# Optimization experiments

Hardware: AMD Instinct MI355X
Metric: run time of the kernel (lower is better)

The kernel has to match this reference:

```python
import jax, jax.numpy as jnp
import numpy as np
from jax import lax

NB_DIGITS = 2
BASE = 10
NUMS = BASE ** NB_DIGITS            # 100 possible values per number
SUMS = 2 * (NUMS - 1) + 1           # 199 possible sums (circuit roots)
B = 4096                            # logical batch size
N_IMAGES = B * 2 * NB_DIGITS        # 16384 digit images


def setup_inputs() -> dict:
    key = jax.random.key(0)
    ks = jax.random.split(key, 11)
    s = 0.1
    return {
        "images": jax.random.normal(ks[0], (N_IMAGES, 1, 28, 28), jnp.float32),
        "conv1_w": jax.random.normal(ks[1], (6, 1, 5, 5), jnp.float32) * s,
        "conv1_b": jax.random.normal(ks[2], (6,), jnp.float32) * s,
        "conv2_w": jax.random.normal(ks[3], (16, 6, 5, 5), jnp.float32) * s,
        "conv2_b": jax.random.normal(ks[4], (16,), jnp.float32) * s,
        "fc1_w": jax.random.normal(ks[5], (120, 256), jnp.float32) * s,
        "fc1_b": jax.random.normal(ks[6], (120,), jnp.float32) * s,
        "fc2_w": jax.random.normal(ks[7], (84, 120), jnp.float32) * s,
        "fc2_b": jax.random.normal(ks[8], (84,), jnp.float32) * s,
        "fc3_w": jax.random.normal(ks[9], (10, 84), jnp.float32) * s,
        "fc3_b": jax.random.normal(ks[10], (10,), jnp.float32) * s,
    }


def _conv(x, w, b):
    y = lax.conv_general_dilated(x, w, (1, 1), 'VALID',
                                 dimension_numbers=('NCHW', 'OIHW', 'NCHW'))
    return y + b[None, :, None, None]


def _maxpool2(x):
    return lax.reduce_window(x, -jnp.inf, lax.max, (1, 1, 2, 2), (1, 1, 2, 2), 'VALID')


def _lenet(x, c1w, c1b, c2w, c2b, f1w, f1b, f2w, f2b, f3w, f3b):
    x = jax.nn.relu(_maxpool2(_conv(x, c1w, c1b)))   # [N,6,12,12]
    x = jax.nn.relu(_maxpool2(_conv(x, c2w, c2b)))   # [N,16,4,4]
    x = x.reshape(-1, 16 * 4 * 4)
    x = jax.nn.relu(x @ f1w.T + f1b)
    x = jax.nn.relu(x @ f2w.T + f2b)
    x = x @ f3w.T + f3b
    return jax.nn.log_softmax(x, axis=-1)            # [N,10]


def _circuit(lp):
    # lp: [B, 2*NB_DIGITS, 10] per-digit log-probs.
    # Vars layout from get_circuit: positions 0..NB_DIGITS-1 = n1 digits (MSB first),
    # positions NB_DIGITS..2*NB_DIGITS-1 = n2 digits. Neg-literal weights are 0 in
    # log space (the `zeros` arg), so each model's weight = sum of digit log-probs;
    # OR over models = logsumexp grouped by n1+n2.
    d = jnp.arange(NUMS)
    hi, lo = d // BASE, d % BASE
    lp1 = lp[:, 0, hi] + lp[:, 1, lo]                # [B, NUMS] log P(n1=k)
    lp2 = lp[:, 2, hi] + lp[:, 3, lo]                # [B, NUMS] log P(n2=k)
    M = (lp1[:, :, None] + lp2[:, None, :]).reshape(lp.shape[0], -1)  # [B, NUMS^2]
    seg = (jnp.arange(NUMS)[:, None] + jnp.arange(NUMS)[None, :]).reshape(-1)
    Mf = M.T                                          # [NUMS^2, B]
    m = jax.ops.segment_max(Mf, seg, num_segments=SUMS)              # [SUMS, B]
    ssum = jax.ops.segment_sum(jnp.exp(Mf - m[seg]), seg, num_segments=SUMS)
    return (jnp.log(ssum) + m).T                      # [B, SUMS] log P(sum=s)


def reference(images, conv1_w, conv1_b, conv2_w, conv2_b,
              fc1_w, fc1_b, fc2_w, fc2_b, fc3_w, fc3_b):
    logp = _lenet(images, conv1_w, conv1_b, conv2_w, conv2_b,
                  fc1_w, fc1_b, fc2_w, fc2_b, fc3_w, fc3_b)   # [N_IMAGES,10]
    lp = logp.reshape(B, 2 * NB_DIGITS, BASE)
    return _circuit(lp)
```

## Files before the change

kernel.cpp:

```cpp
#include <hip/hip_runtime.h>
#include <hip/hip_bf16.h>
#include <math.h>

#define SUMS 199
#define NBLK 1024

typedef __attribute__((ext_vector_type(8))) short short8;
typedef __attribute__((ext_vector_type(4))) float float4v;

union Frag8 { short8 v; unsigned u[4]; uint4 q; };

static __device__ inline unsigned pk_bf16(float a, float b) {
    __hip_bfloat162 h = __float22bfloat162_rn(make_float2(a, b));
    union { __hip_bfloat162 h; unsigned u; } c; c.h = h; return c.u;
}

__global__ __launch_bounds__(256) void convert_weights(
    const float* __restrict__ f1w, const float* __restrict__ f2w,
    const float* __restrict__ f3w, const float* __restrict__ c1w,
    const float* __restrict__ c2w, uint4* __restrict__ ws)
{
    const int g = blockIdx.x * 256 + threadIdx.x;
    if (g >= 6400) return;
    float v[8];
    if (g < 5824) {
        const float* W; int O, K, ld, nt, s, l;
        if (g < 4096)      { W = f1w; O = 120; K = 256; ld = 256; nt = g >> 9; s = (g >> 6) & 7; l = g & 63; }
        else if (g < 5632) { const int f = g - 4096; W = f2w; O = 84; K = 120; ld = 120; nt = f >> 8; s = (f >> 6) & 3; l = f & 63; }
        else               { const int f = g - 5632; W = f3w; O = 10; K = 84;  ld = 84;  nt = 0; s = f >> 6; l = f & 63; }
        const int o = nt * 16 + (l & 15);
        #pragma unroll
        for (int j = 0; j < 8; ++j) {
            const int k = 32 * s + 8 * (l >> 4) + j;
            v[j] = (o < O && k < K) ? W[o * ld + k] : 0.f;
        }
    } else if (g < 6336) {
        const int f = g - 5824, s = f >> 6, l = f & 63;
        const int c = l & 15, h = l >> 4;
        const int pos = 4 * s + h;
        const int ky = pos / 5, kx = pos % 5;
        const bool ok = (pos < 25);
        #pragma unroll
        for (int jp = 0; jp < 4; ++jp) {
            v[2 * jp]     = (ok && 2 * jp < 6)     ? c2w[c * 150 + (2 * jp) * 25 + ky * 5 + kx]     : 0.f;
            v[2 * jp + 1] = (ok && 2 * jp + 1 < 6) ? c2w[c * 150 + (2 * jp + 1) * 25 + ky * 5 + kx] : 0.f;
        }
    } else {
        const int l = (g - 6336) & 63;
        const int c = l & 15, h = l >> 4;
        const int oc = c >> 1, xs = c & 1;
        #pragma unroll
        for (int j = 0; j < 8; ++j) {
            const int p = h * 4 + (j >> 1);
            float w = 0.f;
            if (p < 15 && c < 12) {
                const int ky = p / 3, kx = 2 * (p % 3) + (j & 1) - xs;
                if (kx >= 0 && kx < 5) w = c1w[oc * 25 + ky * 5 + kx];
            }
            v[j] = w;
        }
    }
    uint4 r;
    r.x = pk_bf16(v[0], v[1]); r.y = pk_bf16(v[2], v[3]);
    r.z = pk_bf16(v[4], v[5]); r.w = pk_bf16(v[6], v[7]);
    ws[g] = r;
}

__global__ __launch_bounds__(256, 4) void lenet_circuit_kernel(
    const float* __restrict__ images,
    const float* __restrict__ c1b, const float* __restrict__ c2b,
    const float* __restrict__ f1b, const float* __restrict__ f2b,
    const float* __restrict__ f3b, const uint4* __restrict__ wsb,
    float* __restrict__ out)
{
    __shared__ __align__(16) unsigned char s_mem[39712];
    unsigned*       imgu = (unsigned*)s_mem;
    unsigned short* p1s  = (unsigned short*)(s_mem + 12576);
    const uint4*    p1u4 = (const uint4*)(s_mem + 12576);
    unsigned*       A1d  = (unsigned*)(s_mem + 31264);
    const uint4*    A1q  = (const uint4*)(s_mem + 31264);
    float*          pgf  = (float*)(s_mem + 7680);
    float*          Hf   = (float*)(s_mem + 8448);
    float*          Lf   = (float*)(s_mem + 8768);

    const int t = threadIdx.x, bid = blockIdx.x;
    const int lane = t & 63, wav = t >> 6;
    const int c = lane & 15, h = lane >> 4;
    const uint4 z4 = {0u, 0u, 0u, 0u};

    {
        uint4* pz = (uint4*)(s_mem + 12576);
        for (int i = t; i < 1168; i += 256) pz[i] = z4;
    }
    Frag8 a1; a1.q = wsb[6336 + lane];
    Frag8 w2[7];
    #pragma unroll
    for (int s = 0; s < 7; ++s) w2[s].q = wsb[5824 + s * 64 + lane];
    int koff[7];
    #pragma unroll
    for (int s = 0; s < 7; ++s) {
        const int pos = 4 * s + h;
        koff[s] = (pos < 25) ? (pos / 5) * 12 + (pos % 5) : 0;
    }
    int pd[4];
    #pragma unroll
    for (int q = 0; q < 4; ++q) {
        const int p = 4 * h + q;
        pd[q] = (p < 15) ? (p / 3) * 14 + (p % 3) : 0;
    }
    float bias0 = 0.f, bias1 = 0.f;
    if (h < 3) { bias0 = c1b[2 * h]; bias1 = c1b[2 * h + 1]; }
    const float b2v = c2b[c];

    float4 pf[7];
    {
        const float4* g1 = (const float4*)(images + (size_t)bid * 12544 + 6272);
        #pragma unroll
        for (int k = 0; k < 6; ++k) pf[k] = g1[t + 256 * k];
        if (t < 32) pf[6] = g1[1536 + t];
    }

    auto do_conv1 = [&]() {
        const int n = c, img = n >> 1;
        const int imb = img * 393 + (n & 1) * 14;
        for (int qy = wav * 3; qy < wav * 3 + 3; ++qy) {
            #pragma unroll
            for (int qx = 0; qx < 12; ++qx) {
                const int base = imb + qy * 28 + qx;
                Frag8 bf;
                #pragma unroll
                for (int q = 0; q < 4; ++q) bf.u[q] = imgu[base + pd[q]];
                float4v acc = {0.f, 0.f, 0.f, 0.f};
                acc = __builtin_amdgcn_mfma_f32_16x16x32_bf16(a1.v, bf.v, acc, 0, 0, 0);
                float v0 = fmaxf(acc[0], acc[1]);
                float v1 = fmaxf(acc[2], acc[3]);
                v0 = fmaxf(v0, __shfl_xor(v0, 1));
                v1 = fmaxf(v1, __shfl_xor(v1, 1));
                if ((n & 1) == 0 && h < 3) {
                    const unsigned pkv = pk_bf16(fmaxf(v0 + bias0, 0.f),
                                                 fmaxf(v1 + bias1, 0.f));
                    *(unsigned*)&p1s[img * 1160 + qy * 96 + qx * 8 + 2 * h] = pkv;
                }
            }
        }
    };
    auto do_conv2 = [&](int pass) {
        const int pxl = (c & 1) + 2 * ((c >> 2) & 1);
        const int pyl = ((c >> 1) & 1) + 2 * ((c >> 3) & 1);
        #pragma unroll
        for (int ii = 0; ii < 2; ++ii) {
            const int i0 = 2 * wav + ii;
            #pragma unroll
            for (int mt = 0; mt < 4; ++mt) {
                const int px = pxl + 4 * (mt & 1), py = pyl + 4 * (mt >> 1);
                const int base = i0 * 145 + py * 12 + px;
                float4v acc = {0.f, 0.f, 0.f, 0.f};
                #pragma unroll
                for (int s = 0; s < 7; ++s) {
                    Frag8 af; af.q = p1u4[base + koff[s]];
                    acc = __builtin_amdgcn_mfma_f32_16x16x32_bf16(af.v, w2[s].v, acc, 0, 0, 0);
                }
                const float p = fmaxf(fmaxf(acc[0], acc[1]), fmaxf(acc[2], acc[3]));
                float v = fmaxf(p + b2v, 0.f);
                const float vp = __shfl_xor(v, 16);
                if ((h & 1) == 0) {
                    const int qy = (h >> 1) + 2 * (mt >> 1);
                    A1d[(pass * 8 + i0) * 132 + c * 8 + qy * 2 + (mt & 1)] = pk_bf16(v, vp);
                }
            }
        }
    };

    {
        const float4* g = (const float4*)(images + (size_t)bid * 12544);
        for (int i = t; i < 1568; i += 256) {
            const float4 v = g[i];
            const int im = i / 196, j = i % 196;
            imgu[im * 393 + 2 * j]     = pk_bf16(v.x, v.y);
            imgu[im * 393 + 2 * j + 1] = pk_bf16(v.z, v.w);
        }
    }
    __syncthreads();
    do_conv1();
    __syncthreads();
    do_conv2(0);
    {
        #pragma unroll
        for (int k = 0; k < 6; ++k) {
            const int i = t + 256 * k;
            const int im = i / 196, j = i % 196;
            imgu[im * 393 + 2 * j]     = pk_bf16(pf[k].x, pf[k].y);
            imgu[im * 393 + 2 * j + 1] = pk_bf16(pf[k].z, pf[k].w);
        }
        if (t < 32) {
            const int i = 1536 + t;
            const int im = i / 196, j = i % 196;
            imgu[im * 393 + 2 * j]     = pk_bf16(pf[6].x, pf[6].y);
            imgu[im * 393 + 2 * j + 1] = pk_bf16(pf[6].z, pf[6].w);
        }
    }
    __syncthreads();
    do_conv1();
    __syncthreads();
    do_conv2(1);
    __syncthreads();

    {
        unsigned* A2d = (unsigned*)s_mem;
        if (t < 64) A2d[(t >> 2) * 68 + 60 + (t & 3)] = 0u;
        float4v acc0 = {0.f, 0.f, 0.f, 0.f}, acc1 = acc0;
        const int nt0 = 2 * wav;
        #pragma unroll
        for (int s = 0; s < 8; ++s) {
            Frag8 af; af.q = A1q[c * 33 + 4 * s + h];
            Frag8 b0; b0.q = wsb[(nt0 * 8 + s) * 64 + lane];
            Frag8 b1; b1.q = wsb[((nt0 + 1) * 8 + s) * 64 + lane];
            acc0 = __builtin_amdgcn_mfma_f32_16x16x32_bf16(af.v, b0.v, acc0, 0, 0, 0);
            acc1 = __builtin_amdgcn_mfma_f32_16x16x32_bf16(af.v, b1.v, acc1, 0, 0, 0);
        }
        #pragma unroll
        for (int ntl = 0; ntl < 2; ++ntl) {
            const int o = 32 * wav + 16 * ntl + c;
            const float bias = (o < 120) ? f1b[o] : 0.f;
            #pragma unroll
            for (int r = 0; r < 4; ++r) {
                float v = fmaxf((ntl ? acc1[r] : acc0[r]) + bias, 0.f);
                const float vp = __shfl_xor(v, 1);
                if ((c & 1) == 0 && o < 120)
                    A2d[(4 * h + r) * 68 + (o >> 1)] = pk_bf16(v, vp);
            }
        }
    }
    __syncthreads();

    {
        unsigned* A3d = (unsigned*)(s_mem + 4352);
        if (t < 96) A3d[(t / 6) * 52 + 42 + (t % 6)] = 0u;
        if (wav < 3) {
            const uint4* A2q = (const uint4*)s_mem;
            float4v acc0 = {0.f, 0.f, 0.f, 0.f}, acc1 = acc0;
            const int nt0 = 2 * wav;
            #pragma unroll
            for (int s = 0; s < 4; ++s) {
                Frag8 af; af.q = A2q[c * 17 + 4 * s + h];
                Frag8 b0; b0.q = wsb[4096 + (nt0 * 4 + s) * 64 + lane];
                Frag8 b1; b1.q = wsb[4096 + ((nt0 + 1) * 4 + s) * 64 + lane];
                acc0 = __builtin_amdgcn_mfma_f32_16x16x32_bf16(af.v, b0.v, acc0, 0, 0, 0);
                acc1 = __builtin_amdgcn_mfma_f32_16x16x32_bf16(af.v, b1.v, acc1, 0, 0, 0);
            }
            #pragma unroll
            for (int ntl = 0; ntl < 2; ++ntl) {
                const int o = 32 * wav + 16 * ntl + c;
                const float bias = (o < 84) ? f2b[o] : 0.f;
                #pragma unroll
                for (int r = 0; r < 4; ++r) {
                    float v = fmaxf((ntl ? acc1[r] : acc0[r]) + bias, 0.f);
                    const float vp = __shfl_xor(v, 1);
                    if ((c & 1) == 0 && o < 84)
                        A3d[(4 * h + r) * 52 + (o >> 1)] = pk_bf16(v, vp);
                }
            }
        }
    }
    __syncthreads();

    if (wav == 0) {
        const uint4* A3q = (const uint4*)(s_mem + 4352);
        float4v acc = {0.f, 0.f, 0.f, 0.f};
        #pragma unroll
        for (int s = 0; s < 3; ++s) {
            Frag8 af; af.q = A3q[c * 13 + 4 * s + h];
            Frag8 b; b.q = wsb[5632 + s * 64 + lane];
            acc = __builtin_amdgcn_mfma_f32_16x16x32_bf16(af.v, b.v, acc, 0, 0, 0);
        }
        const float bias = (c < 10) ? f3b[c] : 0.f;
        float x[4], m[4], e[4], sm[4];
        #pragma unroll
        for (int r = 0; r < 4; ++r) {
            x[r] = (c < 10) ? (acc[r] + bias) : -INFINITY;
            m[r] = x[r];
        }
        #pragma unroll
        for (int d = 1; d <= 8; d <<= 1)
            #pragma unroll
            for (int r = 0; r < 4; ++r) m[r] = fmaxf(m[r], __shfl_xor(m[r], d));
        #pragma unroll
        for (int r = 0; r < 4; ++r) { e[r] = (c < 10) ? expf(x[r] - m[r]) : 0.f; sm[r] = e[r]; }
        #pragma unroll
        for (int d = 1; d <= 8; d <<= 1)
            #pragma unroll
            for (int r = 0; r < 4; ++r) sm[r] += __shfl_xor(sm[r], d);
        if (c < 10) {
            #pragma unroll
            for (int r = 0; r < 4; ++r)
                pgf[(4 * h + r) * 12 + c] = e[r] / sm[r];
        }
    }
    __syncthreads();

    if (t < 152) {
        const int be = t / 38, j = t % 38;
        const int isH = (j < 19), b = isH ? j : j - 19;
        const float* pg = pgf + 4 * be * 12;
        const float* PA = pg + (isH ? 0 : 12);
        const float* PB = pg + (isH ? 24 : 36);
        const int ilo = (b > 9) ? b - 9 : 0;
        const int ihi = (b < 9) ? b : 9;
        float s = 0.f;
        for (int i = ilo; i <= ihi; ++i) s += PA[i] * PB[b - i];
        (isH ? Hf : Lf)[be * 20 + b] = s;
    }
    __syncthreads();

    for (int idx = t; idx < 4 * SUMS; idx += 256) {
        const int be = idx / SUMS, s = idx % SUMS;
        const float* H = Hf + be * 20;
        const float* L = Lf + be * 20;
        const int bmin = (s > 18) ? (s - 9) / 10 : 0;
        int bmax = s / 10; if (bmax > 18) bmax = 18;
        float sum = 0.f;
        for (int b = bmin; b <= bmax; ++b) sum += H[b] * L[s - 10 * b];
        out[((size_t)bid * 4 + be) * SUMS + s] = logf(sum);
    }
}

extern "C" void kernel_launch(void* const* d_in, const int* in_sizes, int n_in,
                              void* d_out, int out_size, void* d_ws, size_t ws_size,
                              hipStream_t stream) {
    const float* images = (const float*)d_in[0];
    const float* c1w = (const float*)d_in[1];
    const float* c1b = (const float*)d_in[2];
    const float* c2w = (const float*)d_in[3];
    const float* c2b = (const float*)d_in[4];
    const float* f1w = (const float*)d_in[5];
    const float* f1b = (const float*)d_in[6];
    const float* f2w = (const float*)d_in[7];
    const float* f2b = (const float*)d_in[8];
    const float* f3w = (const float*)d_in[9];
    const float* f3b = (const float*)d_in[10];
    float* out = (float*)d_out;

    convert_weights<<<25, 256, 0, stream>>>(f1w, f2w, f3w, c1w, c2w, (uint4*)d_ws);
    lenet_circuit_kernel<<<NBLK, 256, 0, stream>>>(
        images, c1b, c2b, f1b, f2b, f3b, (const uint4*)d_ws, out);
}
```

Before: 135.4 us.

## Vectorize image staging stores and make circuit tail wave-local without barriers

Image staging in LDS now writes one 8-byte store per float4 instead of two 4-byte stores, using a padded per-image stride of 396 words; the p1 and A1 buffers are shifted to fit. The final fc3/softmax stage now runs redundantly on all four waves, and each wave writes and consumes only its own batch element's probabilities. That lets the two-stage circuit convolution run within each wave without the two block-wide __syncthreads. This trades duplicated MFMA and softmax work for fewer barriers, and relies on wave-local LDS ordering between the writes and the reads.

```diff
diff --git a/kernel.cpp b/kernel.cpp
--- a/kernel.cpp
+++ b/kernel.cpp
@@ -73,12 +73,13 @@
     const float* __restrict__ f3b, const uint4* __restrict__ wsb,
     float* __restrict__ out)
 {
-    __shared__ __align__(16) unsigned char s_mem[39712];
+    __shared__ __align__(16) unsigned char s_mem[39680];
     unsigned*       imgu = (unsigned*)s_mem;
-    unsigned short* p1s  = (unsigned short*)(s_mem + 12576);
-    const uint4*    p1u4 = (const uint4*)(s_mem + 12576);
-    unsigned*       A1d  = (unsigned*)(s_mem + 31264);
-    const uint4*    A1q  = (const uint4*)(s_mem + 31264);
+    uint2*          imgw = (uint2*)s_mem;
+    unsigned short* p1s  = (unsigned short*)(s_mem + 12672);
+    const uint4*    p1u4 = (const uint4*)(s_mem + 12672);
+    unsigned*       A1d  = (unsigned*)(s_mem + 31232);
+    const uint4*    A1q  = (const uint4*)(s_mem + 31232);
     float*          pgf  = (float*)(s_mem + 7680);
     float*          Hf   = (float*)(s_mem + 8448);
     float*          Lf   = (float*)(s_mem + 8768);
@@ -89,8 +90,8 @@
     const uint4 z4 = {0u, 0u, 0u, 0u};
 
     {
-        uint4* pz = (uint4*)(s_mem + 12576);
-        for (int i = t; i < 1168; i += 256) pz[i] = z4;
+        uint4* pz = (uint4*)(s_mem + 12672);
+        for (int i = t; i < 1160; i += 256) pz[i] = z4;
     }
     Frag8 a1; a1.q = wsb[6336 + lane];
     Frag8 w2[7];
@@ -122,7 +123,7 @@
 
     auto do_conv1 = [&]() {
         const int n = c, img = n >> 1;
-        const int imb = img * 393 + (n & 1) * 14;
+        const int imb = img * 396 + (n & 1) * 14;
         for (int qy = wav * 3; qy < wav * 3 + 3; ++qy) {
             #pragma unroll
             for (int qx = 0; qx < 12; ++qx) {
@@ -176,8 +177,8 @@
         for (int i = t; i < 1568; i += 256) {
             const float4 v = g[i];
             const int im = i / 196, j = i % 196;
-            imgu[im * 393 + 2 * j]     = pk_bf16(v.x, v.y);
-            imgu[im * 393 + 2 * j + 1] = pk_bf16(v.z, v.w);
+            uint2 w; w.x = pk_bf16(v.x, v.y); w.y = pk_bf16(v.z, v.w);
+            imgw[im * 198 + j] = w;
         }
     }
     __syncthreads();
@@ -189,14 +190,14 @@
         for (int k = 0; k < 6; ++k) {
             const int i = t + 256 * k;
             const int im = i / 196, j = i % 196;
-            imgu[im * 393 + 2 * j]     = pk_bf16(pf[k].x, pf[k].y);
-            imgu[im * 393 + 2 * j + 1] = pk_bf16(pf[k].z, pf[k].w);
+            uint2 w; w.x = pk_bf16(pf[k].x, pf[k].y); w.y = pk_bf16(pf[k].z, pf[k].w);
+            imgw[im * 198 + j] = w;
         }
         if (t < 32) {
             const int i = 1536 + t;
             const int im = i / 196, j = i % 196;
-            imgu[im * 393 + 2 * j]     = pk_bf16(pf[6].x, pf[6].y);
-            imgu[im * 393 + 2 * j + 1] = pk_bf16(pf[6].z, pf[6].w);
+            uint2 w; w.x = pk_bf16(pf[6].x, pf[6].y); w.y = pk_bf16(pf[6].z, pf[6].w);
+            imgw[im * 198 + j] = w;
         }
     }
     __syncthreads();
@@ -264,7 +265,7 @@
     }
     __syncthreads();
 
-    if (wav == 0) {
+    {
         const uint4* A3q = (const uint4*)(s_mem + 4352);
         float4v acc = {0.f, 0.f, 0.f, 0.f};
         #pragma unroll
@@ -290,37 +291,33 @@
         for (int d = 1; d <= 8; d <<= 1)
             #pragma unroll
             for (int r = 0; r < 4; ++r) sm[r] += __shfl_xor(sm[r], d);
-        if (c < 10) {
+        if (c < 10 && h == wav) {
             #pragma unroll
             for (int r = 0; r < 4; ++r)
-                pgf[(4 * h + r) * 12 + c] = e[r] / sm[r];
-        }
-    }
-    __syncthreads();
-
-    if (t < 152) {
-        const int be = t / 38, j = t % 38;
-        const int isH = (j < 19), b = isH ? j : j - 19;
-        const float* pg = pgf + 4 * be * 12;
-        const float* PA = pg + (isH ? 0 : 12);
-        const float* PB = pg + (isH ? 24 : 36);
-        const int ilo = (b > 9) ? b - 9 : 0;
-        const int ihi = (b < 9) ? b : 9;
-        float s = 0.f;
-        for (int i = ilo; i <= ihi; ++i) s += PA[i] * PB[b - i];
-        (isH ? Hf : Lf)[be * 20 + b] = s;
-    }
-    __syncthreads();
-
-    for (int idx = t; idx < 4 * SUMS; idx += 256) {
-        const int be = idx / SUMS, s = idx % SUMS;
-        const float* H = Hf + be * 20;
-        const float* L = Lf + be * 20;
-        const int bmin = (s > 18) ? (s - 9) / 10 : 0;
-        int bmax = s / 10; if (bmax > 18) bmax = 18;
-        float sum = 0.f;
-        for (int b = bmin; b <= bmax; ++b) sum += H[b] * L[s - 10 * b];
-        out[((size_t)bid * 4 + be) * SUMS + s] = logf(sum);
+                pgf[(4 * wav + r) * 12 + c] = e[r] / sm[r];
+        }
+
+        if (lane < 38) {
+            const int isH = (lane < 19), b = isH ? lane : lane - 19;
+            const float* pg = pgf + 4 * wav * 12;
+            const float* PA = pg + (isH ? 0 : 12);
+            const float* PB = pg + (isH ? 24 : 36);
+            const int ilo = (b > 9) ? b - 9 : 0;
+            const int ihi = (b < 9) ? b : 9;
+            float s = 0.f;
+            for (int i = ilo; i <= ihi; ++i) s += PA[i] * PB[b - i];
+            (isH ? Hf : Lf)[wav * 20 + b] = s;
+        }
+
+        const float* H = Hf + wav * 20;
+        const float* L = Lf + wav * 20;
+        for (int s = lane; s < SUMS; s += 64) {
+            const int bmin = (s > 18) ? (s - 9) / 10 : 0;
+            int bmax = s / 10; if (bmax > 18) bmax = 18;
+            float sum = 0.f;
+            for (int b = bmin; b <= bmax; ++b) sum += H[b] * L[s - 10 * b];
+            out[((size_t)bid * 4 + wav) * SUMS + s] = logf(sum);
+        }
     }
 }
 
```

New measurement: 135.7 us. About the same (+0.2%).
